# Optimization experiments

Measured on AMD Instinct MI355X. Metric: run time of the kernel, lower is better.

The kernel has to match this reference:

```python
import jax, jax.numpy as jnp
import numpy as np

B, S, H, NH = 2, 2048, 4096, 32
HD = H // NH
EPS = 1e-8


def setup_inputs() -> dict:
    key = jax.random.key(0)
    ks = jax.random.split(key, 6)
    return {
        "hidden_states": jax.random.normal(ks[0], (B, S, H), jnp.float32),
        "residual": jax.random.normal(ks[1], (B, S, H), jnp.float32),
        # BLOOM alibi: [batch*num_heads, 1, kv_len]
        "alibi": jax.random.normal(ks[2], (B * NH, 1, S), jnp.float32) * 0.1,
        "attention_mask": jnp.ones((B, S), jnp.bool_),  # unused by this forward path
        "W_qkv": jax.random.normal(ks[3], (3 * H, H), jnp.float32) * (1.0 / np.sqrt(H)),
        "b_qkv": jnp.zeros((3 * H,), jnp.float32),
        "W_dense": jax.random.normal(ks[4], (H, H), jnp.float32) * (1.0 / np.sqrt(H)),
        "b_dense": jnp.zeros((H,), jnp.float32),
    }


def reference(hidden_states, residual, alibi, attention_mask, W_qkv, b_qkv, W_dense, b_dense):
    b, s, h = hidden_states.shape
    nh, hd = NH, h // NH
    inv_norm_factor = 1.0 / np.sqrt(hd)  # attention.inv_norm_factor
    beta = 1.0                            # attention.beta (BLOOM default)

    # fused qkv projection + BLOOM _split_heads: [b, s, nh, 3, hd]
    fused = hidden_states @ W_qkv.T + b_qkv
    fused = fused.reshape(b, s, nh, 3, hd)
    q, k, v = fused[..., 0, :], fused[..., 1, :], fused[..., 2, :]  # each [b, s, nh, hd]
    # The torch permute/reshape round-trips leave reshaped_{q,k,v} = [b, s, nh, hd].

    # offset_key = inv_norm_factor * k + beta * (pinv(Q) * alibi) permuted back
    q_bnsd = jnp.transpose(q, (0, 2, 1, 3))           # [b, nh, s, hd]
    pinv_q = jnp.linalg.pinv(q_bnsd)                   # [b, nh, hd, s]
    alibi4 = alibi.reshape(b, nh, 1, s)                # broadcast over hd
    bias = jnp.transpose(pinv_q * alibi4, (0, 3, 1, 2))  # [b, s, nh, hd]
    offset_k = inv_norm_factor * k + beta * bias

    # memory_efficient_attention on [b, s, nh, hd]: einsum 'b h i d, b h j d' ->
    # attention ACROSS HEADS per sequence position; no mask, no causal, no dropout.
    # Chunked online softmax == single stable softmax with +eps in denominator.
    scale = hd ** -0.5  # q additionally scaled inside memory_efficient_attention
    w = jnp.einsum('bsid,bsjd->bsij', q * scale, offset_k)  # [b, s, nh, nh]
    m = jax.lax.stop_gradient(jnp.max(w, axis=-1, keepdims=True))
    e = jnp.exp(w - m)
    ctx = jnp.einsum('bsij,bsjd->bsid', e, v) / (jnp.sum(e, axis=-1, keepdims=True) + EPS)

    ctx = ctx.reshape(b, s, h)  # flatten(start_dim=2)
    out = ctx @ W_dense.T + b_dense + residual  # dense + dropout_add (eval: p=0)
    return out
```

## Files before the change

kernel.cpp:

```cpp
#include <hip/hip_runtime.h>

#define B_  2
#define S_  2048
#define NH_ 32
#define HD_ 128
#define H_  4096
#define H3_ 12288
#define GP_ 8

typedef __bf16 bf16x8 __attribute__((ext_vector_type(8)));
typedef float  f32x4  __attribute__((ext_vector_type(4)));
typedef float  f32x16 __attribute__((ext_vector_type(16)));

__device__ __forceinline__ unsigned short f2bf(float f) {
  unsigned int u = __float_as_uint(f);
  u += 0x7fffu + ((u >> 16) & 1u);
  return (unsigned short)(u >> 16);
}
__device__ __forceinline__ void unpack8(uint4 r, float f[8]) {
  f[0] = __uint_as_float(r.x << 16); f[1] = __uint_as_float(r.x & 0xffff0000u);
  f[2] = __uint_as_float(r.y << 16); f[3] = __uint_as_float(r.y & 0xffff0000u);
  f[4] = __uint_as_float(r.z << 16); f[5] = __uint_as_float(r.z & 0xffff0000u);
  f[6] = __uint_as_float(r.w << 16); f[7] = __uint_as_float(r.w & 0xffff0000u);
}
__device__ __forceinline__ void gload_lds16(const void* g, void* l) {
  __builtin_amdgcn_global_load_lds(
      (const __attribute__((address_space(1))) unsigned int*)g,
      (__attribute__((address_space(3))) unsigned int*)l, 16, 0, 0);
}

__device__ __forceinline__ void cvt_seg(const float* __restrict__ in,
                                        unsigned short* __restrict__ out,
                                        long n, long base, long stride) {
  for (long i = base; i < n; i += stride) {
    float4 v = *(const float4*)(in + i);
    ushort4 o;
    o.x = f2bf(v.x); o.y = f2bf(v.y); o.z = f2bf(v.z); o.w = f2bf(v.w);
    *(ushort4*)(out + i) = o;
  }
}
__global__ __launch_bounds__(256) void cvt3(
    const float* __restrict__ a, unsigned short* __restrict__ oa, long na,
    const float* __restrict__ b, unsigned short* __restrict__ ob, long nb,
    const float* __restrict__ c, unsigned short* __restrict__ oc, long nc) {
  const long base = ((long)blockIdx.x * 256 + threadIdx.x) * 4;
  const long stride = (long)gridDim.x * 256 * 4;
  cvt_seg(a, oa, na, base, stride);
  cvt_seg(b, ob, nb, base, stride);
  cvt_seg(c, oc, nc, base, stride);
}

template <int EPI>
__global__ __launch_bounds__(512, 2) void gemm256(
    const unsigned short* __restrict__ A, const unsigned short* __restrict__ Bt,
    void* __restrict__ C, const float* __restrict__ bias, const float* __restrict__ Res,
    int lda, int ldb, int ldc, int K)
{
  __shared__ __align__(16) unsigned short lds[3 * 16384];

  const int tid = threadIdx.x;
  const int w = tid >> 6, l = tid & 63;

  const int gx = gridDim.x;
  const int nwg = gx * gridDim.y;
  const int flat = blockIdx.y * gx + blockIdx.x;
  const int swz = (flat & 7) * (nwg >> 3) + (flat >> 3);
  const int m0 = (swz / gx) * 256;
  const int n0 = (swz % gx) * 256;

  const int wr = w >> 2, wc = w & 3;
  const int lr16 = l & 15, kq = l >> 4;

  const int srow = w * 16 + (l >> 2);
  const int scs  = (((l & 3) ^ ((l >> 3) & 3)) << 3);
  const unsigned short* ga = A  + (long)(m0 + srow) * lda + scs;
  const unsigned short* gb = Bt + (long)(n0 + srow) * ldb + scs;
  unsigned short* sb_w = lds + w * 512;

  const int rchunk = ((kq ^ ((l >> 1) & 3)) << 3);

  const int NT = K >> 5;

  const f32x4 zero = {0.f, 0.f, 0.f, 0.f};
  f32x4 acc[8][4];
#pragma unroll
  for (int m = 0; m < 8; ++m)
#pragma unroll
    for (int n = 0; n < 4; ++n) acc[m][n] = zero;

  auto stage = [&](int kt, int s) {
    const unsigned short* a = ga + (long)kt * 32;
    const unsigned short* b = gb + (long)kt * 32;
    unsigned short* d = sb_w + s * 16384;
    gload_lds16(a,                  d);
    gload_lds16(a + 128L * lda,     d + 4096);
    gload_lds16(b,                  d + 8192);
    gload_lds16(b + 128L * ldb,     d + 12288);
  };

  stage(0, 0);
  stage(1, 1);
  asm volatile("s_waitcnt vmcnt(4)" ::: "memory");
  __builtin_amdgcn_s_barrier();

  for (int t = 0; t < NT; ++t) {
    const int cur = t % 3;
    if (t + 2 < NT) stage(t + 2, (t + 2) % 3);

    const unsigned short* sa = lds + cur * 16384;
    const unsigned short* sbB = sa + 8192;
    bf16x8 av[8], bv[4];
#pragma unroll
    for (int n = 0; n < 4; ++n)
      bv[n] = *(const bf16x8*)&sbB[(wc * 64 + n * 16 + lr16) * 32 + rchunk];
#pragma unroll
    for (int m = 0; m < 8; ++m)
      av[m] = *(const bf16x8*)&sa[(wr * 128 + m * 16 + lr16) * 32 + rchunk];

    __builtin_amdgcn_s_setprio(1);
#pragma unroll
    for (int m = 0; m < 8; ++m)
#pragma unroll
      for (int n = 0; n < 4; ++n)
        acc[m][n] = __builtin_amdgcn_mfma_f32_16x16x32_bf16(av[m], bv[n], acc[m][n], 0, 0, 0);
    __builtin_amdgcn_s_setprio(0);

    if (t + 1 < NT) {
      if (t + 2 < NT) asm volatile("s_waitcnt vmcnt(4)" ::: "memory");
      else            asm volatile("s_waitcnt vmcnt(0)" ::: "memory");
      __builtin_amdgcn_s_barrier();
    }
  }

#pragma unroll
  for (int m = 0; m < 8; ++m) {
    const int grow0 = m0 + wr * 128 + m * 16 + kq * 4;
#pragma unroll
    for (int n = 0; n < 4; ++n) {
      const int gcol = n0 + wc * 64 + n * 16 + lr16;
#pragma unroll
      for (int i = 0; i < 4; ++i) {
        const long gi = (long)(grow0 + i) * ldc + gcol;
        float v = acc[m][n][i];
        if (EPI == 0) {
          ((unsigned short*)C)[gi] = f2bf(v + bias[gcol]);
        } else {
          ((float*)C)[gi] = v + bias[gcol] + Res[gi];
        }
      }
    }
  }
}

template <int EPI>
__global__ __launch_bounds__(256) void gemm_bt(
    const unsigned short* __restrict__ Abase, const unsigned short* __restrict__ Bbase,
    void* __restrict__ Cbase, const float* __restrict__ bias, const float* __restrict__ Res,
    int lda, int ldb, int ldc, int K,
    long sAb, long sAn, long sBb, long sBn, long sCb, long sCn)
{
  __shared__ __align__(16) unsigned short As[128][32];
  __shared__ __align__(16) unsigned short Bs[128][32];

  const int zz = blockIdx.z;
  const int zb = zz >> 5, zn = zz & 31;
  const unsigned short* A  = Abase + (long)zb * sAb + (long)zn * sAn;
  const unsigned short* Bm = Bbase + (long)zb * sBb + (long)zn * sBn;
  const long coff = (long)zb * sCb + (long)zn * sCn;

  const int m0 = blockIdx.y * 128;
  const int n0 = blockIdx.x * 128;
  const int tid = threadIdx.x;
  const int wave = tid >> 6;
  const int lane = tid & 63;
  const int wr = wave >> 1, wc = wave & 1;
  const int lr = lane & 15, kq = lane >> 4;
  const int srow = wave * 16 + (lane >> 2);
  const int scol = (((lane & 3) ^ ((lane >> 3) & 3)) << 3);
  const int rch  = ((kq ^ ((lane >> 1) & 3)) << 3);

  const f32x4 zero = {0.0f, 0.0f, 0.0f, 0.0f};
  f32x4 acc[4][4];
#pragma unroll
  for (int m = 0; m < 4; ++m)
#pragma unroll
    for (int n = 0; n < 4; ++n) acc[m][n] = zero;

  for (int k0 = 0; k0 < K; k0 += 32) {
    const unsigned short* ga = A  + (long)(m0 + srow) * lda + k0 + scol;
    const unsigned short* gb = Bm + (long)(n0 + srow) * ldb + k0 + scol;
    gload_lds16(ga,                   &As[wave * 16][0]);
    gload_lds16(ga + (long)64 * lda,  &As[64 + wave * 16][0]);
    gload_lds16(gb,                   &Bs[wave * 16][0]);
    gload_lds16(gb + (long)64 * ldb,  &Bs[64 + wave * 16][0]);
    __syncthreads();

    bf16x8 av[4], bv[4];
#pragma unroll
    for (int m = 0; m < 4; ++m) av[m] = *(const bf16x8*)&As[wr * 64 + m * 16 + lr][rch];
#pragma unroll
    for (int n = 0; n < 4; ++n) bv[n] = *(const bf16x8*)&Bs[wc * 64 + n * 16 + lr][rch];
#pragma unroll
    for (int m = 0; m < 4; ++m)
#pragma unroll
      for (int n = 0; n < 4; ++n)
        acc[m][n] = __builtin_amdgcn_mfma_f32_16x16x32_bf16(av[m], bv[n], acc[m][n], 0, 0, 0);
    __syncthreads();
  }

#pragma unroll
  for (int m = 0; m < 4; ++m) {
    const int grow0 = m0 + wr * 64 + m * 16 + kq * 4;
#pragma unroll
    for (int n = 0; n < 4; ++n) {
      const int gcol = n0 + wc * 64 + n * 16 + lr;
#pragma unroll
      for (int r = 0; r < 4; ++r) {
        const long gi = coff + (long)(grow0 + r) * ldc + gcol;
        float v = acc[m][n][r];
        if (EPI == 0) {
          ((unsigned short*)Cbase)[gi] = f2bf(v + bias[gcol]);
        } else if (EPI == 1) {
          ((float*)Cbase)[gi] = v + bias[gcol] + Res[gi];
        } else {
          ((unsigned short*)Cbase)[gi] = f2bf(v);
        }
      }
    }
  }
}

__global__ __launch_bounds__(256) void compute_g(const unsigned short* __restrict__ fused,
                                                 float* __restrict__ Gpart)
{
  __shared__ __align__(16) unsigned short Qs[64 * 136];
  const int z = blockIdx.x;
  const int b = z >> 5, n = z & 31;
  const unsigned short* Q = fused + (long)b * S_ * H3_ + n * 384;
  const int t = threadIdx.x;
  const int w = t >> 6, l = t & 63;
  const int l31 = l & 31, hi = l >> 5;
  const int ar0 = (w & 1) * 2, ac0 = (w >> 1) * 2;

  f32x16 acc[2][2];
#pragma unroll
  for (int i = 0; i < 2; ++i)
#pragma unroll
    for (int j = 0; j < 2; ++j)
#pragma unroll
      for (int r = 0; r < 16; ++r) acc[i][j][r] = 0.f;

  const int sbeg = blockIdx.y * (S_ / GP_);

  for (int ss0 = 0; ss0 < S_ / GP_; ss0 += 64) {
    __syncthreads();
#pragma unroll
    for (int pass = 0; pass < 4; ++pass) {
      const int sL = pass * 16 + (t >> 4);
      const int c = t & 15;
      uint4 v = *(const uint4*)(Q + (long)(sbeg + ss0 + sL) * H3_ + c * 8);
      *(uint4*)&Qs[sL * 136 + c * 8] = v;
    }
    __syncthreads();

#pragma unroll
    for (int ks = 0; ks < 4; ++ks) {
      const int sb = ks * 16 + hi * 8;
      bf16x8 fa[2], fb[2];
#pragma unroll
      for (int i = 0; i < 2; ++i) {
        const int colA = (ar0 + i) * 32 + l31;
        const int colB = (ac0 + i) * 32 + l31;
        bf16x8 ra, rbv;
#pragma unroll
        for (int j = 0; j < 8; ++j) {
          unsigned short ua = Qs[(sb + j) * 136 + colA];
          unsigned short ub = Qs[(sb + j) * 136 + colB];
          ra[j]  = *reinterpret_cast<__bf16*>(&ua);
          rbv[j] = *reinterpret_cast<__bf16*>(&ub);
        }
        fa[i] = ra; fb[i] = rbv;
      }
#pragma unroll
      for (int i = 0; i < 2; ++i)
#pragma unroll
        for (int j = 0; j < 2; ++j)
          acc[i][j] = __builtin_amdgcn_mfma_f32_32x32x16_bf16(fa[i], fb[j], acc[i][j], 0, 0, 0);
    }
  }

  float* Gp = Gpart + ((long)z * GP_ + blockIdx.y) * 16384;
#pragma unroll
  for (int i = 0; i < 2; ++i) {
    const int rowb = (ar0 + i) * 32 + 4 * hi;
#pragma unroll
    for (int j = 0; j < 2; ++j) {
      const int col = (ac0 + j) * 32 + l31;
#pragma unroll
      for (int r = 0; r < 16; ++r) {
        const int row = rowb + (r & 3) + 8 * (r >> 2);
        Gp[row * 128 + col] = acc[i][j][r];
      }
    }
  }
}

__global__ __launch_bounds__(1024) void invert_g(const float* __restrict__ Gpart,
                                                 unsigned short* __restrict__ Ginv)
{
  __shared__ __align__(16) float prow[2][128];
  __shared__ __align__(16) float pcol[2][128];
  const int z = blockIdx.x;
  const int t = threadIdx.x;
  const int c  = t & 127;
  const int rg = t >> 7;
  const float* Gz = Gpart + (long)z * GP_ * 16384;

  float a[16];
#pragma unroll
  for (int i = 0; i < 16; ++i) {
    const int idx = (rg * 16 + i) * 128 + c;
    float s = 0.f;
#pragma unroll
    for (int p = 0; p < GP_; ++p) s += Gz[p * 16384 + idx];
    a[i] = s;
  }

  for (int p = 0; p < 128; ++p) {
    const int buf = p & 1;
    const int prg = p >> 4, pi = p & 15;
    if (rg == prg) {
      float v = a[0];
#pragma unroll
      for (int i = 1; i < 16; ++i) v = (pi == i) ? a[i] : v;
      prow[buf][c] = v;
    }
    if (c == p) {
#pragma unroll
      for (int q = 0; q < 4; ++q) {
        float4 w4 = make_float4(a[q * 4], a[q * 4 + 1], a[q * 4 + 2], a[q * 4 + 3]);
        *(float4*)&pcol[buf][rg * 16 + q * 4] = w4;
      }
    }
    __syncthreads();
    const float invp = 1.0f / prow[buf][p];
    const float rowv = (c == p) ? invp : prow[buf][c] * invp;
#pragma unroll
    for (int q = 0; q < 4; ++q) {
      const float4 pc4 = *(const float4*)&pcol[buf][rg * 16 + q * 4];
      const float pcv[4] = {pc4.x, pc4.y, pc4.z, pc4.w};
#pragma unroll
      for (int j = 0; j < 4; ++j) {
        const int i = q * 4 + j;
        const int r = rg * 16 + i;
        const float cur = (c == p) ? 0.f : a[i];
        a[i] = (r == p) ? rowv : cur - pcv[j] * rowv;
      }
    }
  }
  unsigned short* Oz = Ginv + (long)z * 16384;
#pragma unroll
  for (int i = 0; i < 16; ++i) Oz[(rg * 16 + i) * 128 + c] = f2bf(a[i]);
}

__global__ __launch_bounds__(256) void attn_pos(
    const unsigned short* __restrict__ fused, const unsigned short* __restrict__ Zb,
    const float* __restrict__ alibi, unsigned short* __restrict__ ctx)
{
  __shared__ __align__(16) unsigned short q_s[32 * 128];
  __shared__ __align__(16) unsigned short v_s[32 * 128];
  __shared__ __align__(16) unsigned short kp[32 * 136];
  __shared__ float wsh[NH_][NH_ + 1];
  __shared__ float pden[NH_];
  __shared__ float alib[NH_];

  const int s = blockIdx.x, b = blockIdx.y;
  const int t = threadIdx.x;
  const int w = t >> 6;
  const unsigned short* src = fused + ((long)b * S_ + s) * H3_;

  if (t < NH_) alib[t] = 0.08838834764831845f * alibi[((long)(b * NH_ + t)) * S_ + s];

  {
    const int i0 = t >> 4, c = t & 15;
    gload_lds16(src + i0 * 384 + c * 8,              (char*)q_s + w * 1024);
    gload_lds16(src + (i0 + 16) * 384 + c * 8,       (char*)q_s + 4096 + w * 1024);
    gload_lds16(src + i0 * 384 + 256 + c * 8,        (char*)v_s + w * 1024);
    gload_lds16(src + (i0 + 16) * 384 + 256 + c * 8, (char*)v_s + 4096 + w * 1024);
  }

  const int kj = t >> 3, kd = (t & 7) * 16;
  const unsigned short* kg = src + kj * 384 + 128 + kd;
  const unsigned short* zg = Zb + ((long)b * S_ + s) * H_ + kj * 128 + kd;
  uint4 kr0 = *(const uint4*)(kg);
  uint4 kr1 = *(const uint4*)(kg + 8);
  uint4 zr0 = *(const uint4*)(zg);
  uint4 zr1 = *(const uint4*)(zg + 8);
  __syncthreads();

  {
    const float aj = alib[kj];
    float kf[16], zf[16];
    unpack8(kr0, kf); unpack8(kr1, kf + 8);
    unpack8(zr0, zf); unpack8(zr1, zf + 8);
    union { uint4 u[2]; unsigned short us[16]; } kk;
#pragma unroll
    for (int d = 0; d < 16; ++d) kk.us[d] = f2bf(0.0078125f * kf[d] + aj * zf[d]);
    *(uint4*)&kp[kj * 136 + kd]     = kk.u[0];
    *(uint4*)&kp[kj * 136 + kd + 8] = kk.u[1];
  }
  __syncthreads();

  const int i = t >> 3;
  const int j0 = (t & 7) * 4;
  const int rot = (i ^ (t & 7)) & 15;
  float wv[4] = {0.f, 0.f, 0.f, 0.f};
  for (int dbi = 0; dbi < 16; ++dbi) {
    const int d0b = ((dbi + rot) & 15) * 8;
    float qf[8];
    unpack8(*(const uint4*)&q_s[i * 128 + d0b], qf);
#pragma unroll
    for (int jj = 0; jj < 4; ++jj) {
      float kf2[8];
      unpack8(*(const uint4*)&kp[(j0 + jj) * 136 + d0b], kf2);
#pragma unroll
      for (int d = 0; d < 8; ++d) wv[jj] += qf[d] * kf2[d];
    }
  }
  float vmax = fmaxf(fmaxf(wv[0], wv[1]), fmaxf(wv[2], wv[3]));
  vmax = fmaxf(vmax, __shfl_xor(vmax, 1));
  vmax = fmaxf(vmax, __shfl_xor(vmax, 2));
  vmax = fmaxf(vmax, __shfl_xor(vmax, 4));
  float ssum = 0.f;
#pragma unroll
  for (int jj = 0; jj < 4; ++jj) { wv[jj] = __expf(wv[jj] - vmax); ssum += wv[jj]; }
#pragma unroll
  for (int jj = 0; jj < 4; ++jj) wsh[i][j0 + jj] = wv[jj];
  ssum += __shfl_xor(ssum, 1);
  ssum += __shfl_xor(ssum, 2);
  ssum += __shfl_xor(ssum, 4);
  if ((t & 7) == 0) pden[i] = 1.0f / (ssum + 1e-8f);
  __syncthreads();

  const int d0 = (t & 7) * 16;
  float acc[16];
#pragma unroll
  for (int d = 0; d < 16; ++d) acc[d] = 0.f;
  for (int j = 0; j < NH_; ++j) {
    const float p = wsh[i][j];
    float vf[16];
    unpack8(*(const uint4*)&v_s[j * 128 + d0], vf);
    unpack8(*(const uint4*)&v_s[j * 128 + d0 + 8], vf + 8);
#pragma unroll
    for (int d = 0; d < 16; ++d) acc[d] += p * vf[d];
  }
  const float inv = pden[i];
  union { uint4 u[2]; unsigned short us[16]; } ov;
#pragma unroll
  for (int d = 0; d < 16; ++d) ov.us[d] = f2bf(acc[d] * inv);
  unsigned short* cp = ctx + ((long)b * S_ + s) * H_ + i * HD_ + d0;
  *(uint4*)&cp[0] = ov.u[0];
  *(uint4*)&cp[8] = ov.u[1];
}

extern "C" void kernel_launch(void* const* d_in, const int* in_sizes, int n_in,
                              void* d_out, int out_size, void* d_ws, size_t ws_size,
                              hipStream_t stream)
{
  (void)in_sizes; (void)n_in; (void)out_size; (void)ws_size;
  const float* hidden   = (const float*)d_in[0];
  const float* residual = (const float*)d_in[1];
  const float* alibi    = (const float*)d_in[2];
  const float* Wqkv     = (const float*)d_in[4];
  const float* bqkv     = (const float*)d_in[5];
  const float* Wd       = (const float*)d_in[6];
  const float* bd       = (const float*)d_in[7];
  float* out = (float*)d_out;

  char* ws = (char*)d_ws;
  size_t off = 0;
  auto carve = [&](size_t bytes) -> void* {
    void* p = ws + off;
    off += (bytes + 255) & ~(size_t)255;
    return p;
  };
  const long nHid = (long)B_ * S_ * H_;
  const long nWq  = (long)H3_ * H_;
  unsigned short* hid_bf   = (unsigned short*)carve((size_t)nHid * 2);
  unsigned short* wqkv_bf  = (unsigned short*)carve((size_t)nWq * 2);
  unsigned short* wd_bf    = (unsigned short*)carve((size_t)H_ * H_ * 2);
  unsigned short* fused_bf = (unsigned short*)carve((size_t)B_ * S_ * H3_ * 2);
  unsigned short* z_bf     = (unsigned short*)carve((size_t)nHid * 2);
  unsigned short* ctx_bf   = (unsigned short*)carve((size_t)nHid * 2);
  float*          Gpart    = (float*)carve((size_t)64 * GP_ * 16384 * 4);
  unsigned short* ginv_bf  = (unsigned short*)carve((size_t)64 * 16384 * 2);

  cvt3<<<2048, 256, 0, stream>>>(hidden, hid_bf, nHid,
                                 Wqkv, wqkv_bf, nWq,
                                 Wd, wd_bf, (long)H_ * H_);

  gemm256<0><<<dim3(H3_ / 256, (B_ * S_) / 256, 1), 512, 0, stream>>>(
      hid_bf, wqkv_bf, fused_bf, bqkv, nullptr, H_, H_, H3_, H_);

  compute_g<<<dim3(64, GP_), 256, 0, stream>>>(fused_bf, Gpart);
  invert_g<<<64, 1024, 0, stream>>>(Gpart, ginv_bf);

  gemm_bt<2><<<dim3(1, S_ / 128, 64), 256, 0, stream>>>(
      fused_bf, ginv_bf, z_bf, nullptr, nullptr, H3_, HD_, H_, HD_,
      (long)S_ * H3_, 384, (long)32 * 16384, 16384, (long)S_ * H_, HD_);

  attn_pos<<<dim3(S_, B_), 256, 0, stream>>>(fused_bf, z_bf, alibi, ctx_bf);

  gemm256<1><<<dim3(H_ / 256, (B_ * S_) / 256, 1), 512, 0, stream>>>(
      ctx_bf, wd_bf, out, bd, residual, H_, H_, H_, H_);
}
```

Measured before the change: 792.7 us.

## Compute per-position head-score matrix with MFMA instead of scalar dot products

The 32x32 per-position attention score matrix (q against offset key) is now computed with bf16 MFMA 32x32x16 instructions. The K and Z terms are multiplied separately and combined algebraically (scale*QK + alibi*QZ), instead of first building a bf16 offset-key tile and doing scalar FMA loops. The head dimension is split across the four waves, and their partial results are reduced through shared memory. This adds LDS usage (extra k/z tiles and a partial buffer) plus another barrier. Precision changes slightly because the offset key is no longer rounded to bf16 before the product.

```diff
diff --git a/kernel.cpp b/kernel.cpp
--- a/kernel.cpp
+++ b/kernel.cpp
@@ -367,66 +367,78 @@
     const unsigned short* __restrict__ fused, const unsigned short* __restrict__ Zb,
     const float* __restrict__ alibi, unsigned short* __restrict__ ctx)
 {
-  __shared__ __align__(16) unsigned short q_s[32 * 128];
+  __shared__ __align__(16) unsigned short q_s[32 * 136];
+  __shared__ __align__(16) unsigned short k_s[32 * 136];
+  __shared__ __align__(16) unsigned short z_s[32 * 136];
   __shared__ __align__(16) unsigned short v_s[32 * 128];
-  __shared__ __align__(16) unsigned short kp[32 * 136];
+  __shared__ float part[4][32][33];
   __shared__ float wsh[NH_][NH_ + 1];
   __shared__ float pden[NH_];
   __shared__ float alib[NH_];
 
   const int s = blockIdx.x, b = blockIdx.y;
   const int t = threadIdx.x;
-  const int w = t >> 6;
+  const int w = t >> 6, l = t & 63;
+  const int l31 = l & 31, hi = l >> 5;
   const unsigned short* src = fused + ((long)b * S_ + s) * H3_;
+  const unsigned short* zg = Zb + ((long)b * S_ + s) * H_;
 
   if (t < NH_) alib[t] = 0.08838834764831845f * alibi[((long)(b * NH_ + t)) * S_ + s];
 
   {
     const int i0 = t >> 4, c = t & 15;
-    gload_lds16(src + i0 * 384 + c * 8,              (char*)q_s + w * 1024);
-    gload_lds16(src + (i0 + 16) * 384 + c * 8,       (char*)q_s + 4096 + w * 1024);
     gload_lds16(src + i0 * 384 + 256 + c * 8,        (char*)v_s + w * 1024);
     gload_lds16(src + (i0 + 16) * 384 + 256 + c * 8, (char*)v_s + 4096 + w * 1024);
   }
-
-  const int kj = t >> 3, kd = (t & 7) * 16;
-  const unsigned short* kg = src + kj * 384 + 128 + kd;
-  const unsigned short* zg = Zb + ((long)b * S_ + s) * H_ + kj * 128 + kd;
-  uint4 kr0 = *(const uint4*)(kg);
-  uint4 kr1 = *(const uint4*)(kg + 8);
-  uint4 zr0 = *(const uint4*)(zg);
-  uint4 zr1 = *(const uint4*)(zg + 8);
+  {
+    const int row = t >> 3, c = (t & 7) * 16;
+    uint4 a0 = *(const uint4*)(src + row * 384 + c);
+    uint4 a1 = *(const uint4*)(src + row * 384 + c + 8);
+    uint4 b0 = *(const uint4*)(src + row * 384 + 128 + c);
+    uint4 b1 = *(const uint4*)(src + row * 384 + 128 + c + 8);
+    uint4 c0 = *(const uint4*)(zg + row * 128 + c);
+    uint4 c1 = *(const uint4*)(zg + row * 128 + c + 8);
+    *(uint4*)&q_s[row * 136 + c] = a0; *(uint4*)&q_s[row * 136 + c + 8] = a1;
+    *(uint4*)&k_s[row * 136 + c] = b0; *(uint4*)&k_s[row * 136 + c + 8] = b1;
+    *(uint4*)&z_s[row * 136 + c] = c0; *(uint4*)&z_s[row * 136 + c + 8] = c1;
+  }
   __syncthreads();
 
   {
-    const float aj = alib[kj];
-    float kf[16], zf[16];
-    unpack8(kr0, kf); unpack8(kr1, kf + 8);
-    unpack8(zr0, zf); unpack8(zr1, zf + 8);
-    union { uint4 u[2]; unsigned short us[16]; } kk;
-#pragma unroll
-    for (int d = 0; d < 16; ++d) kk.us[d] = f2bf(0.0078125f * kf[d] + aj * zf[d]);
-    *(uint4*)&kp[kj * 136 + kd]     = kk.u[0];
-    *(uint4*)&kp[kj * 136 + kd + 8] = kk.u[1];
+    f32x16 g1, g2;
+#pragma unroll
+    for (int r = 0; r < 16; ++r) { g1[r] = 0.f; g2[r] = 0.f; }
+#pragma unroll
+    for (int ks = 0; ks < 2; ++ks) {
+      const int off = w * 32 + ks * 16 + hi * 8;
+      bf16x8 aq = *(const bf16x8*)&q_s[l31 * 136 + off];
+      bf16x8 bk = *(const bf16x8*)&k_s[l31 * 136 + off];
+      bf16x8 bz = *(const bf16x8*)&z_s[l31 * 136 + off];
+      g1 = __builtin_amdgcn_mfma_f32_32x32x16_bf16(aq, bk, g1, 0, 0, 0);
+      g2 = __builtin_amdgcn_mfma_f32_32x32x16_bf16(aq, bz, g2, 0, 0, 0);
+    }
+    const float aj = alib[l31];
+#pragma unroll
+    for (int r = 0; r < 16; ++r) {
+      const int row = (r & 3) + 8 * (r >> 2) + 4 * hi;
+      part[w][row][l31] = 0.0078125f * g1[r] + aj * g2[r];
+    }
+  }
+  __syncthreads();
+
+#pragma unroll
+  for (int e = 0; e < 4; ++e) {
+    const int idx = t * 4 + e;
+    const int ii = idx >> 5, jj = idx & 31;
+    wsh[ii][jj] = part[0][ii][jj] + part[1][ii][jj] + part[2][ii][jj] + part[3][ii][jj];
   }
   __syncthreads();
 
   const int i = t >> 3;
   const int j0 = (t & 7) * 4;
-  const int rot = (i ^ (t & 7)) & 15;
-  float wv[4] = {0.f, 0.f, 0.f, 0.f};
-  for (int dbi = 0; dbi < 16; ++dbi) {
-    const int d0b = ((dbi + rot) & 15) * 8;
-    float qf[8];
-    unpack8(*(const uint4*)&q_s[i * 128 + d0b], qf);
-#pragma unroll
-    for (int jj = 0; jj < 4; ++jj) {
-      float kf2[8];
-      unpack8(*(const uint4*)&kp[(j0 + jj) * 136 + d0b], kf2);
-#pragma unroll
-      for (int d = 0; d < 8; ++d) wv[jj] += qf[d] * kf2[d];
-    }
-  }
+  float wv[4];
+#pragma unroll
+  for (int jj = 0; jj < 4; ++jj) wv[jj] = wsh[i][j0 + jj];
   float vmax = fmaxf(fmaxf(wv[0], wv[1]), fmaxf(wv[2], wv[3]));
   vmax = fmaxf(vmax, __shfl_xor(vmax, 1));
   vmax = fmaxf(vmax, __shfl_xor(vmax, 2));
```

Result: faster. 775.1 us (-2.2%).
